# Optimization experiments

Hardware: AMD Instinct MI355X
Metric: run time of the kernel (lower is better)

Reference implementation:

```python
import jax, jax.numpy as jnp
import numpy as np

HIDDEN = 1024
NUM_HEADS = 16
HEAD = HIDDEN // NUM_HEADS
B, S = 2, 2048


def setup_inputs() -> dict:
    key = jax.random.key(0)
    ks = jax.random.split(key, 7)
    scale = 1.0 / np.sqrt(HIDDEN)
    return {
        "hidden_states": jax.random.normal(ks[0], (B, S, HIDDEN), dtype=jnp.float32),
        "Wq": jax.random.normal(ks[1], (HIDDEN, HIDDEN), dtype=jnp.float32) * scale,
        "bq": jax.random.normal(ks[2], (HIDDEN,), dtype=jnp.float32) * 0.01,
        "Wk": jax.random.normal(ks[3], (HIDDEN, HIDDEN), dtype=jnp.float32) * scale,
        "bk": jax.random.normal(ks[4], (HIDDEN,), dtype=jnp.float32) * 0.01,
        "Wv": jax.random.normal(ks[5], (HIDDEN, HIDDEN), dtype=jnp.float32) * scale,
        "bv": jax.random.normal(ks[6], (HIDDEN,), dtype=jnp.float32) * 0.01,
    }


def _split_heads(x):
    b, s, _ = x.shape
    return x.reshape(b, s, NUM_HEADS, HEAD).transpose(0, 2, 1, 3)  # [B,H,S,D]


def reference(hidden_states, Wq, bq, Wk, bk, Wv, bv):
    # Linear projections (dropout is inference no-op)
    Q = _split_heads(hidden_states @ Wq + bq)
    K = _split_heads(hidden_states @ Wk + bk)
    V = _split_heads(hidden_states @ Wv + bv)
    scores = jnp.einsum("bhqd,bhkd->bhqk", Q, K) / np.sqrt(HEAD).astype(np.float32)
    probs = jax.nn.softmax(scores, axis=-1)
    context = jnp.einsum("bhqk,bhkd->bhqd", probs, V)  # [B,H,S,D]
    return context.transpose(0, 2, 1, 3).reshape(B, S, HIDDEN)
```

## Files before the change

### kernel.cpp

```cpp
#include <hip/hip_runtime.h>
#include <hip/hip_bf16.h>

typedef __bf16 bf16_t;
typedef __bf16 bf16x4v __attribute__((ext_vector_type(4)));
typedef __bf16 bf16x8 __attribute__((ext_vector_type(8)));
typedef float f32x4 __attribute__((ext_vector_type(4)));
typedef float f32x16 __attribute__((ext_vector_type(16)));
typedef unsigned short u16;
typedef unsigned int u32;
typedef u16 u16x8 __attribute__((ext_vector_type(8)));

#define HIDDEN 1024
#define NHEAD 16
#define HEADD 64
#define BATCH 2
#define SEQ 2048
#define TOKENS (BATCH*SEQ)

#define Z16 {0.f,0.f,0.f,0.f,0.f,0.f,0.f,0.f,0.f,0.f,0.f,0.f,0.f,0.f,0.f,0.f}
#define M12F -12.0f
#define M16 {M12F,M12F,M12F,M12F,M12F,M12F,M12F,M12F,M12F,M12F,M12F,M12F,M12F,M12F,M12F,M12F}

__global__ __launch_bounds__(256) void k_transpose_w(const float* __restrict__ Wq,
                                                     const float* __restrict__ Wk,
                                                     const float* __restrict__ Wv,
                                                     bf16_t* __restrict__ wt) {
  int mat = blockIdx.z;
  const float* W = (mat == 0) ? Wq : (mat == 1 ? Wk : Wv);
  bf16_t* dst = wt + (size_t)mat * HIDDEN * HIDDEN;
  __shared__ float tile[32][33];
  int k0 = blockIdx.x * 32, n0 = blockIdx.y * 32;
  int tc = threadIdx.x & 31, tr = threadIdx.x >> 5;
#pragma unroll
  for (int r = 0; r < 32; r += 8)
    tile[tr + r][tc] = W[(size_t)(k0 + tr + r) * HIDDEN + n0 + tc];
  __syncthreads();
#pragma unroll
  for (int r = 0; r < 32; r += 8)
    dst[(size_t)(n0 + tr + r) * HIDDEN + k0 + tc] = (bf16_t)tile[tc][tr + r];
}

__global__ __launch_bounds__(256) void k_gemm_qkv(
    const float* __restrict__ hs, const bf16_t* __restrict__ wt,
    const float* __restrict__ bq, const float* __restrict__ bk,
    const float* __restrict__ bv, bf16_t* __restrict__ Qo,
    bf16_t* __restrict__ Ko, bf16_t* __restrict__ Vo) {
  __shared__ bf16x8 As[2][4 * 128];
  __shared__ bf16x8 Bs[2][4 * 128];
  int t = threadIdx.x;
  int wave = t >> 6, lane = t & 63;
  int m0 = blockIdx.x * 128;
  int nb = blockIdx.y;
  int mat = nb >> 3;
  int n0 = (nb & 7) * 128;
  const bf16_t* Wmat = wt + (size_t)mat * HIDDEN * HIDDEN;
  const float* bias = (mat == 0) ? bq : (mat == 1 ? bk : bv);
  bf16_t* dst = (mat == 0) ? Qo : (mat == 1 ? Ko : Vo);

  int wm = wave >> 1, wn = wave & 1;
  int lrow = lane & 15;
  int lc = lane >> 4;

  f32x4 acc[4][4];
#pragma unroll
  for (int a = 0; a < 4; ++a)
#pragma unroll
    for (int b = 0; b < 4; ++b) acc[a][b] = (f32x4){0.f, 0.f, 0.f, 0.f};

  bf16x8 ra[2], rb[2];
  auto load_tiles = [&](int kt) {
    int k0 = kt * 32;
#pragma unroll
    for (int u = 0; u < 2; ++u) {
      int id = t + u * 256;
      int row = id >> 2, c = id & 3;
      const float* ap = hs + (size_t)(m0 + row) * HIDDEN + k0 + c * 8;
      float4 f0 = *(const float4*)(ap);
      float4 f1 = *(const float4*)(ap + 4);
      bf16x8 v;
      v[0] = (bf16_t)f0.x; v[1] = (bf16_t)f0.y; v[2] = (bf16_t)f0.z; v[3] = (bf16_t)f0.w;
      v[4] = (bf16_t)f1.x; v[5] = (bf16_t)f1.y; v[6] = (bf16_t)f1.z; v[7] = (bf16_t)f1.w;
      ra[u] = v;
      rb[u] = *(const bf16x8*)(Wmat + (size_t)(n0 + row) * HIDDEN + k0 + c * 8);
    }
  };
  auto store_tiles = [&](int buf) {
#pragma unroll
    for (int u = 0; u < 2; ++u) {
      int id = t + u * 256;
      int row = id >> 2, c = id & 3;
      As[buf][c * 128 + (row ^ c)] = ra[u];
      Bs[buf][c * 128 + (row ^ c)] = rb[u];
    }
  };

  load_tiles(0);
  store_tiles(0);
  __syncthreads();
  const int NT = HIDDEN / 32;
  int cur = 0;
  for (int kt = 0; kt < NT; ++kt) {
    if (kt + 1 < NT) load_tiles(kt + 1);
    bf16x8 af[4], bfr[4];
#pragma unroll
    for (int fm = 0; fm < 4; ++fm)
      af[fm] = As[cur][lc * 128 + ((wm * 64 + fm * 16 + lrow) ^ lc)];
#pragma unroll
    for (int fn = 0; fn < 4; ++fn)
      bfr[fn] = Bs[cur][lc * 128 + ((wn * 64 + fn * 16 + lrow) ^ lc)];
#pragma unroll
    for (int fm = 0; fm < 4; ++fm)
#pragma unroll
      for (int fn = 0; fn < 4; ++fn)
        acc[fm][fn] = __builtin_amdgcn_mfma_f32_16x16x32_bf16(
            af[fm], bfr[fn], acc[fm][fn], 0, 0, 0);
    if (kt + 1 < NT) store_tiles(cur ^ 1);
    __syncthreads();
    cur ^= 1;
  }

  float scale = (mat == 0) ? 0.18033688011112042f : 1.0f;
#pragma unroll
  for (int fm = 0; fm < 4; ++fm) {
#pragma unroll
    for (int fn = 0; fn < 4; ++fn) {
      int n = n0 + wn * 64 + fn * 16 + (lane & 15);
      float bval = bias[n];
      int h = n >> 6, d = n & 63;
      int mbase = m0 + wm * 64 + fm * 16 + (lane >> 4) * 4;
      int b = mbase >> 11, s = mbase & 2047;
      if (mat == 2) {
        bf16x4v pk;
#pragma unroll
        for (int j = 0; j < 4; ++j) pk[j] = (bf16_t)(acc[fm][fn][j] + bval);
        *(bf16x4v*)(dst + ((size_t)(b * NHEAD + h) * HEADD + d) * SEQ + s) = pk;
      } else {
#pragma unroll
        for (int j = 0; j < 4; ++j) {
          float v = (acc[fm][fn][j] + bval) * scale;
          dst[((size_t)(b * NHEAD + h) * SEQ + (s + j)) * HEADD + d] = (bf16_t)v;
        }
      }
    }
  }
}

__device__ __forceinline__ void gload16(const void* g, void* l) {
  __builtin_amdgcn_global_load_lds((const __attribute__((address_space(1))) u32*)g,
                                   (__attribute__((address_space(3))) u32*)l, 16, 0, 0);
}

__global__ __launch_bounds__(512, 4) void k_attn(const bf16_t* __restrict__ Q,
                                                 const bf16_t* __restrict__ K,
                                                 const bf16_t* __restrict__ Vt,
                                                 float* __restrict__ out) {
  __shared__ __align__(16) char smem[66560];
  const int t = threadIdx.x;
  const int w = t >> 6, l = t & 63;
  const int g = w >> 2, wg = w & 3;
  const int hi = l >> 5;
  const int l31 = l & 31;
  const int lx = l & 7;

  const int n_hw = blockIdx.x + 16 * blockIdx.y;
  const int work = (n_hw & 7) * 64 + (n_hw >> 3);
  const int qt = work & 15;
  const int bh = work >> 4;
  const int b = bh >> 4, h = bh & 15;
  const char* Kp = (const char*)(K + (size_t)bh * SEQ * HEADD) + (size_t)g * 1024 * 128;
  const char* Vp = (const char*)(Vt + (size_t)bh * HEADD * SEQ) + (size_t)g * 1024 * 2;
  const bf16_t* Qp = Q + (size_t)bh * SEQ * HEADD;

  const int q0 = qt * 128 + wg * 32;

  bf16x8 qa[4];
#pragma unroll
  for (int ds = 0; ds < 4; ++ds)
    qa[ds] = *(const bf16x8*)(Qp + (size_t)(q0 + l31) * HEADD + ds * 16 + hi * 8);

  f32x16 o0 = Z16, o1 = Z16;
  float l_run = 0.f;

  char* gK = smem + g * 32768;
  char* gV = gK + 16384;
  const int srow = wg * 16 + (l >> 3);
  const int sg = lx ^ (l >> 3);

  auto stage = [&](int tile, int buf) {
#pragma unroll
    for (int s = 0; s < 2; ++s) {
      int row = srow + 8 * s;
      gload16(Kp + (size_t)(tile * 64 + row) * 128 + sg * 16,
              gK + buf * 8192 + wg * 2048 + s * 1024);
      gload16(Vp + (size_t)row * (SEQ * 2) + tile * 128 + sg * 16,
              gV + buf * 8192 + wg * 2048 + s * 1024);
    }
  };

  stage(0, 0);
  __syncthreads();

  int roff0[4], roff1[4];
#pragma unroll
  for (int ds = 0; ds < 4; ++ds) {
    roff0[ds] = l31 * 128 + ((2 * ds + hi) ^ lx) * 16;
    roff1[ds] = (32 + l31) * 128 + ((2 * ds + hi) ^ lx) * 16;
  }

  int cur = 0;
  for (int r = 0; r < 16; ++r) {
    if (r < 15) stage(r + 1, cur ^ 1);
    const char* Kc = gK + cur * 8192;
    const char* Vc = gV + cur * 8192;

    f32x16 s0 = M16, s1 = M16;
    __builtin_amdgcn_s_setprio(1);
#pragma unroll
    for (int ds = 0; ds < 4; ++ds) {
      bf16x8 kf0 = *(const bf16x8*)(Kc + roff0[ds]);
      s0 = __builtin_amdgcn_mfma_f32_32x32x16_bf16(kf0, qa[ds], s0, 0, 0, 0);
      bf16x8 kf1 = *(const bf16x8*)(Kc + roff1[ds]);
      s1 = __builtin_amdgcn_mfma_f32_32x32x16_bf16(kf1, qa[ds], s1, 0, 0, 0);
    }
    __builtin_amdgcn_s_setprio(0);

#pragma unroll
    for (int i = 0; i < 16; ++i) {
      s0[i] = __builtin_amdgcn_exp2f(s0[i]);
      s1[i] = __builtin_amdgcn_exp2f(s1[i]);
    }
    {
      float ta[16];
#pragma unroll
      for (int i = 0; i < 16; ++i) ta[i] = s0[i] + s1[i];
#pragma unroll
      for (int i = 0; i < 8; ++i) ta[i] += ta[i + 8];
#pragma unroll
      for (int i = 0; i < 4; ++i) ta[i] += ta[i + 4];
      l_run += (ta[0] + ta[1]) + (ta[2] + ta[3]);
    }

    bf16x8 pf[4];
    {
      u32 u[16];
#pragma unroll
      for (int i = 0; i < 8; ++i) {
        union { bf16_t h[2]; u32 ww; } c0, c1;
        c0.h[0] = (bf16_t)s0[2 * i]; c0.h[1] = (bf16_t)s0[2 * i + 1];
        c1.h[0] = (bf16_t)s1[2 * i]; c1.h[1] = (bf16_t)s1[2 * i + 1];
        u[i] = c0.ww; u[8 + i] = c1.ww;
      }
#pragma unroll
      for (int gg = 0; gg < 4; ++gg) {
        u32 a0 = u[4 * gg + 0], b0 = u[4 * gg + 2];
        u32 a1 = u[4 * gg + 1], b1 = u[4 * gg + 3];
        asm("v_permlane32_swap_b32 %0, %1" : "+v"(a0), "+v"(b0));
        asm("v_permlane32_swap_b32 %0, %1" : "+v"(a1), "+v"(b1));
        union { u32 wv[4]; bf16x8 v; } fu;
        fu.wv[0] = a0; fu.wv[1] = a1; fu.wv[2] = b0; fu.wv[3] = b1;
        pf[gg] = fu.v;
      }
    }

    __builtin_amdgcn_s_setprio(1);
#pragma unroll
    for (int kblk = 0; kblk < 4; ++kblk) {
      bf16x8 vf0 = *(const bf16x8*)(Vc + roff0[kblk]);
      o0 = __builtin_amdgcn_mfma_f32_32x32x16_bf16(vf0, pf[kblk], o0, 0, 0, 0);
      bf16x8 vf1 = *(const bf16x8*)(Vc + roff1[kblk]);
      o1 = __builtin_amdgcn_mfma_f32_32x32x16_bf16(vf1, pf[kblk], o1, 0, 0, 0);
    }
    __builtin_amdgcn_s_setprio(0);
    __syncthreads();
    cur ^= 1;
  }

  float l_half = l_run + __shfl_xor(l_run, 32);
  float* OL = (float*)(smem + g * 32768);
  const int orow = wg * 32 + l31;
#pragma unroll
  for (int j = 0; j < 16; ++j) {
    int dv0 = (j & 3) + 8 * (j >> 2) + 4 * hi;
    OL[orow * 64 + ((dv0 + orow) & 63)] = o0[j];
    int dv1 = 32 + dv0;
    OL[orow * 64 + ((dv1 + orow) & 63)] = o1[j];
  }
  float* LL = (float*)(smem + 65536);
  if (hi == 0) LL[g * 128 + orow] = l_half;
  __syncthreads();
  {
    int ql = t >> 2;
    int dvb = (t & 3) * 16;
    float inv = 1.0f / (LL[ql] + LL[128 + ql]);
    const float* A0 = (const float*)smem;
    const float* B0 = (const float*)(smem + 32768);
    float* op = out + ((size_t)b * SEQ + qt * 128 + ql) * HIDDEN + h * HEADD + dvb;
#pragma unroll
    for (int g4 = 0; g4 < 4; ++g4) {
      f32x4 v4;
#pragma unroll
      for (int e = 0; e < 4; ++e) {
        int dv = dvb + g4 * 4 + e;
        int idx = ql * 64 + ((dv + ql) & 63);
        v4[e] = (A0[idx] + B0[idx]) * inv;
      }
      *(f32x4*)(op + g4 * 4) = v4;
    }
  }
}

extern "C" void kernel_launch(void* const* d_in, const int* in_sizes, int n_in,
                              void* d_out, int out_size, void* d_ws, size_t ws_size,
                              hipStream_t stream) {
  const float* hs = (const float*)d_in[0];
  const float* Wq = (const float*)d_in[1];
  const float* bq = (const float*)d_in[2];
  const float* Wk = (const float*)d_in[3];
  const float* bk = (const float*)d_in[4];
  const float* Wv = (const float*)d_in[5];
  const float* bv = (const float*)d_in[6];
  float* out = (float*)d_out;
  char* ws = (char*)d_ws;

  const size_t SZ_X = (size_t)TOKENS * HIDDEN * 2;
  const size_t SZ_W = (size_t)3 * HIDDEN * HIDDEN * 2;
  const size_t SZ_P = (size_t)TOKENS * HIDDEN * 2;
  bf16_t* Wt = (bf16_t*)(ws + SZ_X);
  bf16_t* Qb = (bf16_t*)(ws + SZ_X + SZ_W);
  bf16_t* Kb = (bf16_t*)(ws + SZ_X + SZ_W + SZ_P);
  bf16_t* Vb = (bf16_t*)(ws + SZ_X + SZ_W + 2 * SZ_P);

  k_transpose_w<<<dim3(32, 32, 3), 256, 0, stream>>>(Wq, Wk, Wv, Wt);
  k_gemm_qkv<<<dim3(32, 24), 256, 0, stream>>>(hs, Wt, bq, bk, bv, Qb, Kb, Vb);
  k_attn<<<dim3(16, 32), 512, 0, stream>>>(Qb, Kb, Vb, out);
}
```

Baseline: 104.6 us.

## Software-pipeline attention so QK of the next tile overlaps softmax and PV

Restructures the attention main loop into a two-stage software pipeline. The QK^T MFMAs for tile r+1 are issued alongside the exp/sum/pack and PV MFMAs for tile r, so matrix work and vector work can interleave. K stays double-buffered while V becomes triple-buffered in LDS, which grows shared memory from about 65KB to 80KB. The cost is two live score accumulator sets per wave, which raises register pressure and could cause spills under the 512-thread launch bound.

```diff
diff --git a/kernel.cpp b/kernel.cpp
--- a/kernel.cpp
+++ b/kernel.cpp
@@ -17,7 +17,6 @@
 #define SEQ 2048
 #define TOKENS (BATCH*SEQ)
 
-#define Z16 {0.f,0.f,0.f,0.f,0.f,0.f,0.f,0.f,0.f,0.f,0.f,0.f,0.f,0.f,0.f,0.f}
 #define M12F -12.0f
 #define M16 {M12F,M12F,M12F,M12F,M12F,M12F,M12F,M12F,M12F,M12F,M12F,M12F,M12F,M12F,M12F,M12F}
 
@@ -154,7 +153,7 @@
                                                  const bf16_t* __restrict__ K,
                                                  const bf16_t* __restrict__ Vt,
                                                  float* __restrict__ out) {
-  __shared__ __align__(16) char smem[66560];
+  __shared__ __align__(16) char smem[81920];
   const int t = threadIdx.x;
   const int w = t >> 6, l = t & 63;
   const int g = w >> 2, wg = w & 3;
@@ -178,27 +177,25 @@
   for (int ds = 0; ds < 4; ++ds)
     qa[ds] = *(const bf16x8*)(Qp + (size_t)(q0 + l31) * HEADD + ds * 16 + hi * 8);
 
-  f32x16 o0 = Z16, o1 = Z16;
+  f32x16 o0 = (f32x16)(0.f), o1 = (f32x16)(0.f);
   float l_run = 0.f;
 
-  char* gK = smem + g * 32768;
+  char* gK = smem + g * 40960;
   char* gV = gK + 16384;
   const int srow = wg * 16 + (l >> 3);
   const int sg = lx ^ (l >> 3);
 
-  auto stage = [&](int tile, int buf) {
+  auto stage = [&](int tile) {
+    int kb = tile & 1, vb = tile % 3;
 #pragma unroll
     for (int s = 0; s < 2; ++s) {
       int row = srow + 8 * s;
       gload16(Kp + (size_t)(tile * 64 + row) * 128 + sg * 16,
-              gK + buf * 8192 + wg * 2048 + s * 1024);
+              gK + kb * 8192 + wg * 2048 + s * 1024);
       gload16(Vp + (size_t)row * (SEQ * 2) + tile * 128 + sg * 16,
-              gV + buf * 8192 + wg * 2048 + s * 1024);
-    }
-  };
-
-  stage(0, 0);
-  __syncthreads();
+              gV + vb * 8192 + wg * 2048 + s * 1024);
+    }
+  };
 
   int roff0[4], roff1[4];
 #pragma unroll
@@ -207,47 +204,47 @@
     roff1[ds] = (32 + l31) * 128 + ((2 * ds + hi) ^ lx) * 16;
   }
 
-  int cur = 0;
-  for (int r = 0; r < 16; ++r) {
-    if (r < 15) stage(r + 1, cur ^ 1);
-    const char* Kc = gK + cur * 8192;
-    const char* Vc = gV + cur * 8192;
-
-    f32x16 s0 = M16, s1 = M16;
+  const f32x16 minit = M16;
+
+  auto qk_tile = [&](int kb, f32x16& d0, f32x16& d1) {
+    const char* Kc = gK + kb * 8192;
+    d0 = minit; d1 = minit;
     __builtin_amdgcn_s_setprio(1);
 #pragma unroll
     for (int ds = 0; ds < 4; ++ds) {
       bf16x8 kf0 = *(const bf16x8*)(Kc + roff0[ds]);
-      s0 = __builtin_amdgcn_mfma_f32_32x32x16_bf16(kf0, qa[ds], s0, 0, 0, 0);
+      d0 = __builtin_amdgcn_mfma_f32_32x32x16_bf16(kf0, qa[ds], d0, 0, 0, 0);
       bf16x8 kf1 = *(const bf16x8*)(Kc + roff1[ds]);
-      s1 = __builtin_amdgcn_mfma_f32_32x32x16_bf16(kf1, qa[ds], s1, 0, 0, 0);
+      d1 = __builtin_amdgcn_mfma_f32_32x32x16_bf16(kf1, qa[ds], d1, 0, 0, 0);
     }
     __builtin_amdgcn_s_setprio(0);
-
+  };
+
+  auto sm_pv = [&](int vb, f32x16& p0, f32x16& p1) {
+    const char* Vc = gV + vb * 8192;
 #pragma unroll
     for (int i = 0; i < 16; ++i) {
-      s0[i] = __builtin_amdgcn_exp2f(s0[i]);
-      s1[i] = __builtin_amdgcn_exp2f(s1[i]);
+      p0[i] = __builtin_amdgcn_exp2f(p0[i]);
+      p1[i] = __builtin_amdgcn_exp2f(p1[i]);
     }
     {
       float ta[16];
 #pragma unroll
-      for (int i = 0; i < 16; ++i) ta[i] = s0[i] + s1[i];
+      for (int i = 0; i < 16; ++i) ta[i] = p0[i] + p1[i];
 #pragma unroll
       for (int i = 0; i < 8; ++i) ta[i] += ta[i + 8];
 #pragma unroll
       for (int i = 0; i < 4; ++i) ta[i] += ta[i + 4];
       l_run += (ta[0] + ta[1]) + (ta[2] + ta[3]);
     }
-
     bf16x8 pf[4];
     {
       u32 u[16];
 #pragma unroll
       for (int i = 0; i < 8; ++i) {
         union { bf16_t h[2]; u32 ww; } c0, c1;
-        c0.h[0] = (bf16_t)s0[2 * i]; c0.h[1] = (bf16_t)s0[2 * i + 1];
-        c1.h[0] = (bf16_t)s1[2 * i]; c1.h[1] = (bf16_t)s1[2 * i + 1];
+        c0.h[0] = (bf16_t)p0[2 * i]; c0.h[1] = (bf16_t)p0[2 * i + 1];
+        c1.h[0] = (bf16_t)p1[2 * i]; c1.h[1] = (bf16_t)p1[2 * i + 1];
         u[i] = c0.ww; u[8 + i] = c1.ww;
       }
 #pragma unroll
@@ -261,7 +258,6 @@
         pf[gg] = fu.v;
       }
     }
-
     __builtin_amdgcn_s_setprio(1);
 #pragma unroll
     for (int kblk = 0; kblk < 4; ++kblk) {
@@ -271,9 +267,31 @@
       o1 = __builtin_amdgcn_mfma_f32_32x32x16_bf16(vf1, pf[kblk], o1, 0, 0, 0);
     }
     __builtin_amdgcn_s_setprio(0);
+  };
+
+  f32x16 A0, A1, B0, B1;
+  stage(0);
+  __syncthreads();
+  stage(1);
+  qk_tile(0, A0, A1);
+  __syncthreads();
+  stage(2);
+  qk_tile(1, B0, B1);
+  sm_pv(0, A0, A1);
+  __syncthreads();
+#pragma unroll 1
+  for (int rr = 2; rr < 15; rr += 2) {
+    stage(rr + 1);
+    qk_tile(rr & 1, A0, A1);
+    sm_pv((rr - 1) % 3, B0, B1);
     __syncthreads();
-    cur ^= 1;
-  }
+    if (rr + 2 < 16) stage(rr + 2);
+    qk_tile((rr + 1) & 1, B0, B1);
+    sm_pv(rr % 3, A0, A1);
+    __syncthreads();
+  }
+  sm_pv(15 % 3, B0, B1);
+  __syncthreads();
 
   float l_half = l_run + __shfl_xor(l_run, 32);
   float* OL = (float*)(smem + g * 32768);
@@ -292,8 +310,8 @@
     int ql = t >> 2;
     int dvb = (t & 3) * 16;
     float inv = 1.0f / (LL[ql] + LL[128 + ql]);
-    const float* A0 = (const float*)smem;
-    const float* B0 = (const float*)(smem + 32768);
+    const float* A = (const float*)smem;
+    const float* B = (const float*)(smem + 32768);
     float* op = out + ((size_t)b * SEQ + qt * 128 + ql) * HIDDEN + h * HEADD + dvb;
 #pragma unroll
     for (int g4 = 0; g4 < 4; ++g4) {
@@ -302,7 +320,7 @@
       for (int e = 0; e < 4; ++e) {
         int dv = dvb + g4 * 4 + e;
         int idx = ql * 64 + ((dv + ql) & 63);
-        v4[e] = (A0[idx] + B0[idx]) * inv;
+        v4[e] = (A[idx] + B[idx]) * inv;
       }
       *(f32x4*)(op + g4 * 4) = v4;
     }
```

Result: slower. 161.5 us (+54.3%).
